# Performance work log

Hardware: AMD Instinct MI355X
Metric: run time of the kernel (lower is better)

The kernel has to match this reference:

```python
import jax, jax.numpy as jnp
import numpy as np

N_VERTS = 5000
N_FACES = 10000
BATCH = 2
N_PTS = 8192
OUTER_LOOP = 4
INNER_LOOP = 50
SOLVE_SCALE = 10.0
ADAM_LR = 0.01
B1, B2, EPS = 0.9, 0.999, 1e-8


def _normalize(x, eps=1e-12):
    # torch.nn.functional.normalize(p=2, dim=-1)
    n = jnp.linalg.norm(x, axis=-1, keepdims=True)
    return x / jnp.maximum(n, eps)


def _interp_bary(tri, vw):
    # tri: [M,3,3] per-point triangle attributes, vw: [M,2] barycentric (u,v)
    bary = jnp.concatenate([vw, 1.0 - vw[:, :1] - vw[:, 1:2]], axis=-1)  # [M,3]
    return jnp.einsum('mij,mi->mj', tri, bary)


def _solve_delta_vwd(qV, fid, vw, mesh_V, mesh_F, mesh_N):
    # Newton-like correspondence solve via unrolled Adam (solve_delta_vwd).
    tri_idx = mesh_F[fid]          # [M,3]
    tri_V = mesh_V[tri_idx]        # [M,3,3]
    tri_N = mesh_N[tri_idx]        # [M,3,3]
    d0 = jnp.linalg.norm(_interp_bary(tri_V, vw) - qV, axis=-1)
    delta0 = jnp.concatenate([jnp.zeros_like(vw), d0[:, None]], axis=-1)  # [M,3]
    target = qV * SOLVE_SCALE

    def loss_fn(delta):
        w = vw + delta[:, :2]
        cV = _interp_bary(tri_V, w) * SOLVE_SCALE
        cN = _normalize(_interp_bary(tri_N, w)) * SOLVE_SCALE
        match = cV + cN * delta[:, 2:3]
        return jnp.mean((match - target) ** 2)  # F.mse_loss

    def step(carry, t):
        delta, m, v = carry
        g = jax.grad(loss_fn)(delta)
        m = B1 * m + (1.0 - B1) * g
        v = B2 * v + (1.0 - B2) * g * g
        mhat = m / (1.0 - B1 ** t)
        vhat = v / (1.0 - B2 ** t)
        delta = delta - ADAM_LR * mhat / (jnp.sqrt(vhat) + EPS)
        return (delta, m, v), None

    ts = jnp.arange(1, INNER_LOOP + 1, dtype=qV.dtype)
    zeros = jnp.zeros_like(delta0)
    (delta, _, _), _ = jax.lax.scan(step, (delta0, zeros, zeros), ts)
    return delta


def _forward(verts, mesh_V, mesh_N, mesh_F):
    b, n, _ = verts.shape
    # init_corres_spt: KNN (K=1) of query points against triangle centers
    centers = mesh_V[mesh_F].mean(axis=1)  # [F,3]
    d2 = ((verts ** 2).sum(-1)[..., None]
          + (centers ** 2).sum(-1)[None, None, :]
          - 2.0 * jnp.einsum('bnd,fd->bnf', verts, centers))  # [b,n,F]
    fidx = jnp.argmin(d2, axis=-1)                             # [b,n]
    fid = fidx.reshape(-1)
    qV = verts.reshape(-1, 3)
    vw = jnp.full((b * n, 2), 1.0 / 3.0, dtype=verts.dtype)
    # update_corres_spt (method='uvd'): outer triwalk loop.
    # triwalk is an external CPU mesh-walker; we use the module's documented
    # fallback when triwalk is None: vw <- vw + delta (face index unchanged).
    for _ in range(OUTER_LOOP):
        delta = _solve_delta_vwd(qV, fid, vw, mesh_V, mesh_F, mesh_N)
        vw = vw + delta[:, :2]
    outlier_mask = jnp.zeros((b, n), dtype=bool)  # max_dist = inf
    return fidx, vw.reshape(b, n, 2), outlier_mask


def setup_inputs() -> dict:
    key = jax.random.key(0)
    k1, k2, k3, k4 = jax.random.split(key, 4)
    mesh_V = jax.random.normal(k1, (N_VERTS, 3), dtype=jnp.float32)
    mesh_F = jax.random.randint(k2, (N_FACES, 3), 0, N_VERTS)
    mesh_N = _normalize(jax.random.normal(k3, (N_VERTS, 3), dtype=jnp.float32))
    verts = jax.random.normal(k4, (BATCH, N_PTS, 3), dtype=jnp.float32)
    return {"verts": verts, "mesh_V": mesh_V, "mesh_N": mesh_N, "mesh_F": mesh_F}


def reference(verts, mesh_V, mesh_N, mesh_F):
    return _forward(verts, mesh_V, mesh_N, mesh_F)
```

## Files before the change

kernel.cpp:

```cpp
#include <hip/hip_runtime.h>
#include <math.h>
#include <stdint.h>

constexpr int kVerts = 5000;
constexpr int kFaces = 10000;
constexpr int kPts   = 16384;
constexpr int kOuter = 4;
constexpr int kInner = 50;

#define SCALE 10.0f

#define KNN_WAVES 16
#define KNN_FQ    4
constexpr int kQuarter     = kFaces / KNN_FQ;
constexpr int kPairs       = kQuarter / 2;
constexpr int kPtsPerLane  = 2;
constexpr int kPtsPerBlock = 64 * kPtsPerLane;
constexpr int kPtGroups    = kPts / kPtsPerBlock;

typedef float v2f __attribute__((ext_vector_type(2)));

__device__ __forceinline__ v2f pk_mul(v2f a, v2f b) {
    v2f d; asm("v_pk_mul_f32 %0, %1, %2" : "=v"(d) : "v"(a), "v"(b)); return d;
}
__device__ __forceinline__ v2f pk_add(v2f a, v2f b) {
    v2f d; asm("v_pk_add_f32 %0, %1, %2" : "=v"(d) : "v"(a), "v"(b)); return d;
}

struct BiasTabP { float rb[kInner + 2][2]; };
constexpr BiasTabP make_tabp() {
    BiasTabP t{};
    float b1 = 1.0f, b2 = 1.0f;
    for (int i = 0; i < kInner; ++i) {
        b1 *= 0.9f; b2 *= 0.999f;
        t.rb[i][0] = 1.0f / (1.0f - b1);
        t.rb[i][1] = 1.0f / (1.0f - b2);
    }
    t.rb[kInner][0]     = t.rb[kInner - 1][0];
    t.rb[kInner][1]     = t.rb[kInner - 1][1];
    t.rb[kInner + 1][0] = t.rb[kInner - 1][0];
    t.rb[kInner + 1][1] = t.rb[kInner - 1][1];
    return t;
}
constexpr BiasTabP kTabP = make_tabp();

__global__ __launch_bounds__(256)
void centers_kernel(const float* __restrict__ mesh_V,
                    const int*   __restrict__ mesh_F,
                    float*       __restrict__ soa)
{
    const int f = blockIdx.x * 256 + threadIdx.x;
    if (f >= kFaces) return;
    const int i0 = mesh_F[f * 3 + 0];
    const int i1 = mesh_F[f * 3 + 1];
    const int i2 = mesh_F[f * 3 + 2];
    const float cx = __fdiv_rn(__fadd_rn(__fadd_rn(mesh_V[i0*3+0], mesh_V[i1*3+0]), mesh_V[i2*3+0]), 3.0f);
    const float cy = __fdiv_rn(__fadd_rn(__fadd_rn(mesh_V[i0*3+1], mesh_V[i1*3+1]), mesh_V[i2*3+1]), 3.0f);
    const float cz = __fdiv_rn(__fadd_rn(__fadd_rn(mesh_V[i0*3+2], mesh_V[i1*3+2]), mesh_V[i2*3+2]), 3.0f);
    const float cc = __fadd_rn(__fadd_rn(__fmul_rn(cx, cx), __fmul_rn(cy, cy)),
                               __fmul_rn(cz, cz));
    soa[0 * kFaces + f] = cx;
    soa[1 * kFaces + f] = cy;
    soa[2 * kFaces + f] = cz;
    soa[3 * kFaces + f] = cc;
}

__global__ __launch_bounds__(1024, 8)
void knn_kernel(const float* __restrict__ verts,
                const float* __restrict__ soa,
                float*       __restrict__ ws_d2,
                int*         __restrict__ ws_f)
{
    __shared__ float4 s_A[kPairs];
    __shared__ float4 s_B[kPairs];
    __shared__ float  s_best [KNN_WAVES][kPtsPerBlock];
    __shared__ int    s_bestf[KNN_WAVES][kPtsPerBlock];

    const int tid  = threadIdx.x;
    const int lane = tid & 63;
    const int wv   = __builtin_amdgcn_readfirstlane(tid >> 6);
    const int pg   = blockIdx.x >> 2;
    const int fq   = blockIdx.x & 3;
    const int qbeg = fq * kQuarter;

    for (int p = tid; p < kPairs; p += 1024) {
        const v2f cx2 = *reinterpret_cast<const v2f*>(soa + 0 * kFaces + qbeg + 2 * p);
        const v2f cy2 = *reinterpret_cast<const v2f*>(soa + 1 * kFaces + qbeg + 2 * p);
        const v2f cz2 = *reinterpret_cast<const v2f*>(soa + 2 * kFaces + qbeg + 2 * p);
        const v2f cc2 = *reinterpret_cast<const v2f*>(soa + 3 * kFaces + qbeg + 2 * p);
        s_A[p] = make_float4(cx2.x, cx2.y, cy2.x, cy2.y);
        s_B[p] = make_float4(cz2.x, cz2.y, cc2.x, cc2.y);
    }

    v2f ndx[kPtsPerLane], ndy[kPtsPerLane], ndz[kPtsPerLane], q2p[kPtsPerLane];
#pragma unroll
    for (int k = 0; k < kPtsPerLane; ++k) {
        const int p = pg * kPtsPerBlock + k * 64 + lane;
        const float qx = verts[p * 3 + 0];
        const float qy = verts[p * 3 + 1];
        const float qz = verts[p * 3 + 2];
        const float q2 = __fadd_rn(__fadd_rn(__fmul_rn(qx, qx), __fmul_rn(qy, qy)),
                                   __fmul_rn(qz, qz));
        const float nx = -__fmul_rn(2.0f, qx);
        const float ny = -__fmul_rn(2.0f, qy);
        const float nz = -__fmul_rn(2.0f, qz);
        ndx[k] = (v2f){nx, nx};  asm("" : "+v"(ndx[k]));
        ndy[k] = (v2f){ny, ny};  asm("" : "+v"(ndy[k]));
        ndz[k] = (v2f){nz, nz};  asm("" : "+v"(ndz[k]));
        q2p[k] = (v2f){q2, q2};  asm("" : "+v"(q2p[k]));
    }

    float bd0[kPtsPerLane], bd1[kPtsPerLane];
    int   bf0[kPtsPerLane], bf1[kPtsPerLane];
#pragma unroll
    for (int k = 0; k < kPtsPerLane; ++k) {
        bd0[k] = INFINITY;   bd1[k] = INFINITY;
        bf0[k] = 0x7fffffff; bf1[k] = 0x7fffffff;
    }

    __syncthreads();

    const int pbeg = (wv * kPairs) / KNN_WAVES;
    const int pend = ((wv + 1) * kPairs) / KNN_WAVES;

#pragma unroll 2
    for (int f = pbeg; f < pend; ++f) {
        const float4 ab = s_A[f];
        const float4 zb = s_B[f];
        const v2f cx2 = (v2f){ab.x, ab.y};
        const v2f cy2 = (v2f){ab.z, ab.w};
        const v2f cz2 = (v2f){zb.x, zb.y};
        const v2f cc2 = (v2f){zb.z, zb.w};
        const int gf  = qbeg + 2 * f;
#pragma unroll
        for (int k = 0; k < kPtsPerLane; ++k) {
            const v2f m0   = pk_mul(ndx[k], cx2);
            const v2f m1   = pk_mul(ndy[k], cy2);
            const v2f m2   = pk_mul(ndz[k], cz2);
            const v2f s01  = pk_add(m0, m1);
            const v2f dotn = pk_add(s01, m2);
            const v2f qc   = pk_add(q2p[k], cc2);
            const v2f d2   = pk_add(qc, dotn);
            if (d2.x < bd0[k]) { bd0[k] = d2.x; bf0[k] = gf; }
            if (d2.y < bd1[k]) { bd1[k] = d2.y; bf1[k] = gf + 1; }
        }
    }

#pragma unroll
    for (int k = 0; k < kPtsPerLane; ++k) {
        if (bd1[k] < bd0[k] || (bd1[k] == bd0[k] && bf1[k] < bf0[k])) {
            bd0[k] = bd1[k]; bf0[k] = bf1[k];
        }
        s_best [wv][k * 64 + lane] = bd0[k];
        s_bestf[wv][k * 64 + lane] = bf0[k];
    }
    __syncthreads();

    if (tid < kPtsPerBlock) {
        float best  = s_best [0][tid];
        int   bestf = s_bestf[0][tid];
#pragma unroll
        for (int w = 1; w < KNN_WAVES; ++w) {
            const float ob = s_best [w][tid];
            const int   of = s_bestf[w][tid];
            if (ob < best || (ob == best && of < bestf)) { best = ob; bestf = of; }
        }
        const int p = pg * kPtsPerBlock + tid;
        ws_d2[fq * kPts + p] = best;
        ws_f [fq * kPts + p] = bestf;
    }
}

template<int K>
__device__ __forceinline__ float qbcast(float v) {
    return __int_as_float(__builtin_amdgcn_update_dpp(
        0, __float_as_int(v), K * 0x55 , 0xF, 0xF, true));
}

__global__ __launch_bounds__(256)
void solve_kernel(const float* __restrict__ verts,
                  const float* __restrict__ mesh_V,
                  const float* __restrict__ mesh_N,
                  const int*   __restrict__ mesh_F,
                  const float* __restrict__ ws_d2,
                  const int*   __restrict__ ws_f,
                  float*       __restrict__ out)
{
    const int t  = blockIdx.x * 256 + threadIdx.x;
    const int p  = t >> 2;
    const int ch = t & 3;
    const bool isV = (ch == 1);
    const bool isD = (ch >= 2);

    float bdm = ws_d2[p];
    int   f   = ws_f[p];
#pragma unroll
    for (int q = 1; q < KNN_FQ; ++q) {
        const float d  = ws_d2[q * kPts + p];
        const int   ff = ws_f [q * kPts + p];
        if (d < bdm) { bdm = d; f = ff; }
    }
    if (ch == 0) out[p] = (float)f;

    const float qx = verts[p * 3 + 0];
    const float qy = verts[p * 3 + 1];
    const float qz = verts[p * 3 + 2];

    const int i0 = mesh_F[f * 3 + 0];
    const int i1 = mesh_F[f * 3 + 1];
    const int i2 = mesh_F[f * 3 + 2];

    const float V0x = mesh_V[i0*3+0], V0y = mesh_V[i0*3+1], V0z = mesh_V[i0*3+2];
    const float V1x = mesh_V[i1*3+0], V1y = mesh_V[i1*3+1], V1z = mesh_V[i1*3+2];
    const float V2x = mesh_V[i2*3+0], V2y = mesh_V[i2*3+1], V2z = mesh_V[i2*3+2];
    const float N0x = mesh_N[i0*3+0], N0y = mesh_N[i0*3+1], N0z = mesh_N[i0*3+2];
    const float N1x = mesh_N[i1*3+0], N1y = mesh_N[i1*3+1], N1z = mesh_N[i1*3+2];
    const float N2x = mesh_N[i2*3+0], N2y = mesh_N[i2*3+1], N2z = mesh_N[i2*3+2];

    const float E0x = V0x - V2x, E0y = V0y - V2y, E0z = V0z - V2z;
    const float E1x = V1x - V2x, E1y = V1y - V2y, E1z = V1z - V2z;
    const float F0x = N0x - N2x, F0y = N0y - N2y, F0z = N0z - N2z;
    const float F1x = N1x - N2x, F1y = N1y - N2y, F1z = N1z - N2z;

    const float Aux = isV ? E1x : E0x;
    const float Auy = isV ? E1y : E0y;
    const float Auz = isV ? E1z : E0z;
    const float Bx  = isD ? 0.0f : (isV ? F1x : F0x);
    const float By  = isD ? 0.0f : (isV ? F1y : F0y);
    const float Bz  = isD ? 0.0f : (isV ? F1z : F0z);

    const float tx = qx * SCALE, ty = qy * SCALE, tz = qz * SCALE;
    const float GS = 2.0f / (3.0f * 16384.0f);
    const float B1c = 0.9f,  ONE_M_B1 = 1.0f - 0.9f;
    const float B2c = 0.999f, ONE_M_B2 = 1.0f - 0.999f;

    float vwu = 1.0f / 3.0f, vwv = 1.0f / 3.0f;

#define SOLVE_STEP(RB1, RB2)                                                   \
    {                                                                          \
        const float du = qbcast<0>(dlt);                                       \
        const float dv = qbcast<1>(dlt);                                       \
        const float dd = qbcast<2>(dlt);                                       \
        const float bu = vwu + du;                                             \
        const float bv = vwv + dv;                                             \
        const float bw = (1.0f - bu) - bv;                                     \
        const float cVx = ((bu * V0x + bv * V1x) + bw * V2x) * SCALE;          \
        const float cVy = ((bu * V0y + bv * V1y) + bw * V2y) * SCALE;          \
        const float cVz = ((bu * V0z + bv * V1z) + bw * V2z) * SCALE;          \
        const float nrx = (bu * N0x + bv * N1x) + bw * N2x;                    \
        const float nry = (bu * N0y + bv * N1y) + bw * N2y;                    \
        const float nrz = (bu * N0z + bv * N1z) + bw * N2z;                    \
        const float nn  = (nrx * nrx + nry * nry) + nrz * nrz;                 \
        const float inv = __builtin_amdgcn_rsqf(nn);                           \
        const float nhx = nrx * inv, nhy = nry * inv, nhz = nrz * inv;         \
        const float cNx = nhx * SCALE, cNy = nhy * SCALE, cNz = nhz * SCALE;   \
        const float rx = (cVx + cNx * dd) - tx;                                \
        const float ry = (cVy + cNy * dd) - ty;                                \
        const float rz = (cVz + cNz * dd) - tz;                                \
        const float Ax = isD ? nhx : Aux;                                      \
        const float Ay = isD ? nhy : Auy;                                      \
        const float Az = isD ? nhz : Auz;                                      \
        const float dotA = (rx * Ax + ry * Ay) + rz * Az;                      \
        const float dotB = (rx * Bx + ry * By) + rz * Bz;                      \
        const float nhB  = (nhx * Bx + nhy * By) + nhz * Bz;                   \
        const float nr_r = qbcast<2>(dotA);                                    \
        const float g = GS * (SCALE * dotA + (dd * SCALE) * ((dotB - nr_r * nhB) * inv)); \
        mA = B1c * mA + ONE_M_B1 * g;                                          \
        vA = B2c * vA + ONE_M_B2 * (g * g);                                    \
        const float s = __builtin_amdgcn_rsqf(vA * (RB2) + 1e-16f);            \
        dlt -= 0.01f * (mA * (RB1)) * s;                                       \
    }

    for (int outer = 0; outer < kOuter; ++outer) {
        const float bw0 = (1.0f - vwu) - vwv;
        const float px = ((vwu * V0x + vwv * V1x) + bw0 * V2x);
        const float py = ((vwu * V0y + vwv * V1y) + bw0 * V2y);
        const float pz = ((vwu * V0z + vwv * V1z) + bw0 * V2z);
        const float dx = px - qx, dy = py - qy, dz = pz - qz;
        const float d0 = __builtin_amdgcn_sqrtf((dx * dx + dy * dy) + dz * dz);

        float dlt = isD ? d0 : 0.0f;
        float mA  = 0.0f, vA = 0.0f;

        float rbA1 = kTabP.rb[0][0], rbA2 = kTabP.rb[0][1];
        float rbB1 = kTabP.rb[1][0], rbB2 = kTabP.rb[1][1];
#pragma unroll 1
        for (int it2 = 0; it2 < kInner / 2; ++it2) {
            const float n1a = kTabP.rb[2 * it2 + 2][0];
            const float n2a = kTabP.rb[2 * it2 + 2][1];
            const float n1b = kTabP.rb[2 * it2 + 3][0];
            const float n2b = kTabP.rb[2 * it2 + 3][1];
            SOLVE_STEP(rbA1, rbA2);
            SOLVE_STEP(rbB1, rbB2);
            rbA1 = n1a; rbA2 = n2a; rbB1 = n1b; rbB2 = n2b;
        }
        vwu += qbcast<0>(dlt);
        vwv += qbcast<1>(dlt);
    }
#undef SOLVE_STEP

    if (ch == 0) {
        out[kPts + 2 * p + 0] = vwu;
        out[kPts + 2 * p + 1] = vwv;
        out[3 * kPts + p]     = 0.0f;
    }
}

extern "C" void kernel_launch(void* const* d_in, const int* in_sizes, int n_in,
                              void* d_out, int out_size, void* d_ws, size_t ws_size,
                              hipStream_t stream) {
    const float* verts  = (const float*)d_in[0];
    const float* mesh_V = (const float*)d_in[1];
    const float* mesh_N = (const float*)d_in[2];
    const int*   mesh_F = (const int*)d_in[3];
    float* out = (float*)d_out;

    float* ws_soa = (float*)d_ws;
    float* ws_d2  = (float*)((char*)d_ws + 4 * kFaces * sizeof(float));
    int*   ws_f   = (int*)((char*)ws_d2 + KNN_FQ * kPts * sizeof(float));

    hipLaunchKernelGGL(centers_kernel, dim3((kFaces + 255) / 256), dim3(256), 0, stream,
                       mesh_V, mesh_F, ws_soa);
    hipLaunchKernelGGL(knn_kernel,     dim3(kPtGroups * KNN_FQ), dim3(1024), 0, stream,
                       verts, ws_soa, ws_d2, ws_f);
    hipLaunchKernelGGL(solve_kernel,   dim3(kPts * 4 / 256), dim3(256), 0, stream,
                       verts, mesh_V, mesh_N, mesh_F, ws_d2, ws_f, out);
}
```

Before: 128.0 us.

## Drop per-point norm from KNN distance and retile faces into eighths

The KNN inner loop no longer adds the query's squared norm, since it is constant per point and does not change the argmin. This removes one packed add per face pair. The face range is split into eight segments instead of four, and each lane now handles four points instead of two, so every LDS load of face data is reused across more points. The solve kernel merges eight partial minima instead of four. Hand-written packed-math inline asm is replaced by vector-type arithmetic with FP contraction disabled; this relies on the compiler emitting packed ops itself. Leaving out q2 may change rounding and tie-breaking relative to the reference distance.

```diff
diff --git a/kernel.cpp b/kernel.cpp
--- a/kernel.cpp
+++ b/kernel.cpp
@@ -11,21 +11,14 @@
 #define SCALE 10.0f
 
 #define KNN_WAVES 16
-#define KNN_FQ    4
-constexpr int kQuarter     = kFaces / KNN_FQ;
-constexpr int kPairs       = kQuarter / 2;
-constexpr int kPtsPerLane  = 2;
+#define KNN_SEG   8
+constexpr int kEighth      = kFaces / KNN_SEG;
+constexpr int kPairsE      = kEighth / 2;
+constexpr int kPtsPerLane  = 4;
 constexpr int kPtsPerBlock = 64 * kPtsPerLane;
 constexpr int kPtGroups    = kPts / kPtsPerBlock;
 
 typedef float v2f __attribute__((ext_vector_type(2)));
-
-__device__ __forceinline__ v2f pk_mul(v2f a, v2f b) {
-    v2f d; asm("v_pk_mul_f32 %0, %1, %2" : "=v"(d) : "v"(a), "v"(b)); return d;
-}
-__device__ __forceinline__ v2f pk_add(v2f a, v2f b) {
-    v2f d; asm("v_pk_add_f32 %0, %1, %2" : "=v"(d) : "v"(a), "v"(b)); return d;
-}
 
 struct BiasTabP { float rb[kInner + 2][2]; };
 constexpr BiasTabP make_tabp() {
@@ -71,19 +64,19 @@
                 float*       __restrict__ ws_d2,
                 int*         __restrict__ ws_f)
 {
-    __shared__ float4 s_A[kPairs];
-    __shared__ float4 s_B[kPairs];
+    __shared__ float4 s_A[kPairsE];
+    __shared__ float4 s_B[kPairsE];
     __shared__ float  s_best [KNN_WAVES][kPtsPerBlock];
     __shared__ int    s_bestf[KNN_WAVES][kPtsPerBlock];
 
     const int tid  = threadIdx.x;
     const int lane = tid & 63;
     const int wv   = __builtin_amdgcn_readfirstlane(tid >> 6);
-    const int pg   = blockIdx.x >> 2;
-    const int fq   = blockIdx.x & 3;
-    const int qbeg = fq * kQuarter;
-
-    for (int p = tid; p < kPairs; p += 1024) {
+    const int pg   = blockIdx.x >> 3;
+    const int fq   = blockIdx.x & 7;
+    const int qbeg = fq * kEighth;
+
+    for (int p = tid; p < kPairsE; p += 1024) {
         const v2f cx2 = *reinterpret_cast<const v2f*>(soa + 0 * kFaces + qbeg + 2 * p);
         const v2f cy2 = *reinterpret_cast<const v2f*>(soa + 1 * kFaces + qbeg + 2 * p);
         const v2f cz2 = *reinterpret_cast<const v2f*>(soa + 2 * kFaces + qbeg + 2 * p);
@@ -92,22 +85,19 @@
         s_B[p] = make_float4(cz2.x, cz2.y, cc2.x, cc2.y);
     }
 
-    v2f ndx[kPtsPerLane], ndy[kPtsPerLane], ndz[kPtsPerLane], q2p[kPtsPerLane];
+    v2f ndx[kPtsPerLane], ndy[kPtsPerLane], ndz[kPtsPerLane];
 #pragma unroll
     for (int k = 0; k < kPtsPerLane; ++k) {
         const int p = pg * kPtsPerBlock + k * 64 + lane;
         const float qx = verts[p * 3 + 0];
         const float qy = verts[p * 3 + 1];
         const float qz = verts[p * 3 + 2];
-        const float q2 = __fadd_rn(__fadd_rn(__fmul_rn(qx, qx), __fmul_rn(qy, qy)),
-                                   __fmul_rn(qz, qz));
         const float nx = -__fmul_rn(2.0f, qx);
         const float ny = -__fmul_rn(2.0f, qy);
         const float nz = -__fmul_rn(2.0f, qz);
         ndx[k] = (v2f){nx, nx};  asm("" : "+v"(ndx[k]));
         ndy[k] = (v2f){ny, ny};  asm("" : "+v"(ndy[k]));
         ndz[k] = (v2f){nz, nz};  asm("" : "+v"(ndz[k]));
-        q2p[k] = (v2f){q2, q2};  asm("" : "+v"(q2p[k]));
     }
 
     float bd0[kPtsPerLane], bd1[kPtsPerLane];
@@ -120,8 +110,8 @@
 
     __syncthreads();
 
-    const int pbeg = (wv * kPairs) / KNN_WAVES;
-    const int pend = ((wv + 1) * kPairs) / KNN_WAVES;
+    const int pbeg = (wv * kPairsE) / KNN_WAVES;
+    const int pend = ((wv + 1) * kPairsE) / KNN_WAVES;
 
 #pragma unroll 2
     for (int f = pbeg; f < pend; ++f) {
@@ -134,15 +124,15 @@
         const int gf  = qbeg + 2 * f;
 #pragma unroll
         for (int k = 0; k < kPtsPerLane; ++k) {
-            const v2f m0   = pk_mul(ndx[k], cx2);
-            const v2f m1   = pk_mul(ndy[k], cy2);
-            const v2f m2   = pk_mul(ndz[k], cz2);
-            const v2f s01  = pk_add(m0, m1);
-            const v2f dotn = pk_add(s01, m2);
-            const v2f qc   = pk_add(q2p[k], cc2);
-            const v2f d2   = pk_add(qc, dotn);
-            if (d2.x < bd0[k]) { bd0[k] = d2.x; bf0[k] = gf; }
-            if (d2.y < bd1[k]) { bd1[k] = d2.y; bf1[k] = gf + 1; }
+#pragma clang fp contract(off)
+            const v2f m0   = ndx[k] * cx2;
+            const v2f m1   = ndy[k] * cy2;
+            const v2f m2   = ndz[k] * cz2;
+            const v2f s01  = m0 + m1;
+            const v2f dotn = s01 + m2;
+            const v2f sv   = cc2 + dotn;
+            if (sv.x < bd0[k]) { bd0[k] = sv.x; bf0[k] = gf; }
+            if (sv.y < bd1[k]) { bd1[k] = sv.y; bf1[k] = gf + 1; }
         }
     }
 
@@ -195,7 +185,7 @@
     float bdm = ws_d2[p];
     int   f   = ws_f[p];
 #pragma unroll
-    for (int q = 1; q < KNN_FQ; ++q) {
+    for (int q = 1; q < KNN_SEG; ++q) {
         const float d  = ws_d2[q * kPts + p];
         const int   ff = ws_f [q * kPts + p];
         if (d < bdm) { bdm = d; f = ff; }
@@ -317,11 +307,11 @@
 
     float* ws_soa = (float*)d_ws;
     float* ws_d2  = (float*)((char*)d_ws + 4 * kFaces * sizeof(float));
-    int*   ws_f   = (int*)((char*)ws_d2 + KNN_FQ * kPts * sizeof(float));
+    int*   ws_f   = (int*)((char*)ws_d2 + KNN_SEG * kPts * sizeof(float));
 
     hipLaunchKernelGGL(centers_kernel, dim3((kFaces + 255) / 256), dim3(256), 0, stream,
                        mesh_V, mesh_F, ws_soa);
-    hipLaunchKernelGGL(knn_kernel,     dim3(kPtGroups * KNN_FQ), dim3(1024), 0, stream,
+    hipLaunchKernelGGL(knn_kernel,     dim3(kPtGroups * KNN_SEG), dim3(1024), 0, stream,
                        verts, ws_soa, ws_d2, ws_f);
     hipLaunchKernelGGL(solve_kernel,   dim3(kPts * 4 / 256), dim3(256), 0, stream,
                        verts, mesh_V, mesh_N, mesh_F, ws_d2, ws_f, out);
```

Result: faster. 124.5 us (-2.8%).
